# Kernel optimization log

Measured on AMD Instinct MI355X. Metric: run time of the kernel, lower is better.

## Reference

```python
import jax, jax.numpy as jnp
import numpy as np
from jax import lax

N_CLS = 3
ALPHA = 2
NMS = True


def _make_level(key, B, A, D, H, W, P, counts):
    k1, k2, k3, k4, k5 = jax.random.split(key, 5)
    C = N_CLS * A
    logit = jax.random.normal(k1, (B, C, D, H, W), dtype=jnp.float32)
    # valid positive coords use d,h,w >= 1 so padded writes to (0,0,0,0) never collide
    a = jax.random.randint(k2, (B, P), 0, A)
    d = jax.random.randint(k3, (B, P), 1, D)
    h = jax.random.randint(k4, (B, P), 1, H)
    w = jax.random.randint(k5, (B, P), 1, W)
    labels = jax.random.randint(jax.random.fold_in(key, 7), (B, P), 0, N_CLS)
    valid = jnp.arange(P)[None, :] < jnp.asarray(counts)[:, None]  # [B,P]
    coord = jnp.stack([a, d, h, w], axis=-1)
    coord = jnp.where(valid[..., None], coord, -1).astype(jnp.int32)
    # ground-truth prob map: -1 = negative, class id (float) at positive voxels
    prob_gt = -jnp.ones((B, A, D, H, W), dtype=jnp.float32)
    cs = jnp.where(valid[..., None], coord, 0)
    b_idx = jnp.arange(B)[:, None]
    vals = jnp.where(valid, labels.astype(jnp.float32), -1.0)
    prob_gt = prob_gt.at[b_idx, cs[..., 0], cs[..., 1], cs[..., 2], cs[..., 3]].set(vals)
    return logit, prob_gt, coord


def setup_inputs() -> dict:
    key = jax.random.key(0)
    kA, kB = jax.random.split(key)
    logit0, prob_gt0, coord0 = _make_level(kA, 4, 3, 64, 64, 64, 128, [128, 64, 32, 0])
    logit1, prob_gt1, coord1 = _make_level(kB, 4, 3, 32, 32, 32, 128, [64, 16, 8, 128])
    weight_cls = jnp.array([1.0, 1.5, 2.0], dtype=jnp.float32)
    return {
        "logit0": logit0, "logit1": logit1,
        "prob_gt0": prob_gt0, "prob_gt1": prob_gt1,
        "coord0": coord0, "coord1": coord1,
        "weight_cls": weight_cls,
    }


def _level_loss(logit, prob_gt, coord_gt, weight_cls):
    B, C, D, H, W = logit.shape
    A = C // N_CLS
    logit = logit.reshape(B, N_CLS, A, D, H, W)
    logp = jax.nn.log_softmax(logit, axis=1)
    nll = -logp                      # [B,N_cls,A,D,H,W]
    prob = jnp.exp(logp)
    nll_neg = nll[:, 0]              # [B,A,D,H,W]
    prob_neg = prob[:, 0]
    negmask = (prob_gt == -1).astype(logit.dtype)
    if NMS:
        mp = lax.reduce_window(nll_neg, -jnp.inf, lax.max,
                               (1, 1, 3, 3, 3), (1, 1, 1, 1, 1),
                               [(0, 0), (0, 0), (1, 1), (1, 1), (1, 1)])
        negmask = negmask * lax.stop_gradient((mp == nll_neg).astype(logit.dtype))
    w_neg = (1.0 - lax.stop_gradient(prob_neg)) ** ALPHA * negmask
    loss_neg = jnp.sum(nll_neg * w_neg)
    count_neg = jnp.sum(w_neg)
    # positives: ragged coord gather, masked instead of per-sample python loop
    valid = coord_gt[:, :, 0] > -1                       # [B,P]
    c = jnp.where(valid[..., None], coord_gt, 0)         # safe coords
    a, d, h, w = c[..., 0], c[..., 1], c[..., 2], c[..., 3]
    b_idx = jnp.arange(B)[:, None]
    cls = prob_gt[b_idx, a, d, h, w].astype(jnp.int32)   # class id at positives
    cls = jnp.where(valid, cls, 0)
    p_t = prob[b_idx, cls, a, d, h, w]
    nll_t = nll[b_idx, cls, a, d, h, w]
    w_pos = ((1.0 - lax.stop_gradient(p_t)) ** ALPHA
             * weight_cls[cls] * valid.astype(logit.dtype))
    loss_pos = jnp.sum(nll_t * w_pos)
    count_pos = jnp.sum(w_pos)
    return loss_pos, loss_neg, count_pos, count_neg


def reference(logit0, logit1, prob_gt0, prob_gt1, coord0, coord1, weight_cls):
    lp0, ln0, cp0, cn0 = _level_loss(logit0, prob_gt0, coord0, weight_cls)
    lp1, ln1, cp1, cn1 = _level_loss(logit1, prob_gt1, coord1, weight_cls)
    return jnp.stack([lp0 + lp1, ln0 + ln1, cp0 + cp1, cn0 + cn1])
```

## Files before the change

kernel.cpp:

```cpp
#include <hip/hip_runtime.h>
#include <math.h>

#define NEG_INF (-INFINITY)

__device__ __forceinline__ float nll3(float l0, float l1, float l2) {
    float m = fmaxf(l0, fmaxf(l1, l2));
    float e0 = __expf(l0 - m);
    float e1 = __expf(l1 - m);
    float e2 = __expf(l2 - m);
    return __logf(e0 + e1 + e2) - (l0 - m);
}

#define S0 262144
#define S1 32768
#define N0 (12 * S0)
#define N1 (12 * S1)
#define N0_4 (N0 / 4)
#define N1_4 (N1 / 4)
#define P1_BLOCKS ((N0_4 + N1_4) / 256)

__global__ __launch_bounds__(256)
void nll_pass(const float* __restrict__ logit0,
              const float* __restrict__ logit1,
              float* __restrict__ nllws) {
    const int idx = blockIdx.x * 256 + threadIdx.x;
    if (idx < N0_4) {
        const int per = S0 / 4;
        const int ba = idx / per, r4 = idx % per;
        const int a = ba % 3, b = ba / 3;
        const float* p = logit0 + ((long)b * 9 + a) * S0 + (long)r4 * 4;
        float4 l0 = *(const float4*)p;
        float4 l1 = *(const float4*)(p + (long)3 * S0);
        float4 l2 = *(const float4*)(p + (long)6 * S0);
        float4 o;
        o.x = nll3(l0.x, l1.x, l2.x);
        o.y = nll3(l0.y, l1.y, l2.y);
        o.z = nll3(l0.z, l1.z, l2.z);
        o.w = nll3(l0.w, l1.w, l2.w);
        *(float4*)(nllws + (long)ba * S0 + (long)r4 * 4) = o;
    } else {
        const int j = idx - N0_4;
        const int per = S1 / 4;
        const int ba = j / per, r4 = j % per;
        const int a = ba % 3, b = ba / 3;
        const float* p = logit1 + ((long)b * 9 + a) * S1 + (long)r4 * 4;
        float4 l0 = *(const float4*)p;
        float4 l1 = *(const float4*)(p + (long)3 * S1);
        float4 l2 = *(const float4*)(p + (long)6 * S1);
        float4 o;
        o.x = nll3(l0.x, l1.x, l2.x);
        o.y = nll3(l0.y, l1.y, l2.y);
        o.z = nll3(l0.z, l1.z, l2.z);
        o.w = nll3(l0.w, l1.w, l2.w);
        *(float4*)(nllws + N0 + (long)ba * S1 + (long)r4 * 4) = o;
    }
}

template<int W, int NR, int TD, int D, int H>
__device__ void nms_strip(int uid, int lane,
                          const float* __restrict__ nlvl,
                          const float* __restrict__ pg,
                          float2* __restrict__ slot) {
    constexpr int LR = W / 4;
    constexpr int NI = NR + 2;
    constexpr int HG = H / NR;
    constexpr int DT = D / TD;
    const int q = lane % LR;
    const int g = lane / LR;

    int t = uid;
    const int hg = t % HG; t /= HG;
    const int dt = t % DT; t /= DT;
    const int ba = t;
    const int h0 = hg * NR, d0 = dt * TD;
    const int HW = H * W;
    const long S = (long)D * HW;
    const float* nb  = nlvl + (long)ba * S;
    const float* pgb = pg + (long)ba * S;

    const int jrow = h0 - 1 + g;
    const bool hv = (jrow >= 0) && (jrow < H) && (g < NI);
    const int hcl = min(max(jrow, 0), H - 1);
    const int rowoff = hcl * W + 4 * q;
    const int prowoff = (h0 + min(g, NR - 1)) * W + 4 * q;

    float4 nl[3]; bool vd[3]; float4 pq[3];
    nl[0] = *(const float4*)(nb + (long)max(d0 - 1, 0) * HW + rowoff);
    vd[0] = (d0 - 1 >= 0);
    nl[1] = *(const float4*)(nb + (long)d0 * HW + rowoff);
    vd[1] = true;
    nl[2] = make_float4(0.f, 0.f, 0.f, 0.f); vd[2] = false;
    pq[0] = pq[1] = pq[2] = make_float4(0.f, 0.f, 0.f, 0.f);

    float vm0[4], vm1[4], cc1[4];
#pragma unroll
    for (int i = 0; i < 4; ++i) { vm0[i] = NEG_INF; vm1[i] = NEG_INF; cc1[i] = 0.f; }

    float loss = 0.f, cnt = 0.f;

#pragma unroll
    for (int s = 0; s <= TD + 1; ++s) {
        if (s <= TD - 1) {
            const int pd = d0 + 1 + s;
            nl[(s + 2) % 3] = *(const float4*)(nb + (long)min(pd, D - 1) * HW + rowoff);
            vd[(s + 2) % 3] = (pd < D);
            pq[s % 3] = *(const float4*)(pgb + (long)(d0 + s) * HW + prowoff);
        }

        const float4 cv = nl[s % 3];
        const bool vv = vd[s % 3] && hv;
        float nvv[4];
        nvv[0] = vv ? cv.x : NEG_INF;
        nvv[1] = vv ? cv.y : NEG_INF;
        nvv[2] = vv ? cv.z : NEG_INF;
        nvv[3] = vv ? cv.w : NEG_INF;

        float le = __shfl(nvv[3], lane - 1);
        float re = __shfl(nvv[0], lane + 1);
        le = (q == 0)      ? NEG_INF : le;
        re = (q == LR - 1) ? NEG_INF : re;
        float rm[4];
        rm[0] = fmaxf(le,     fmaxf(nvv[0], nvv[1]));
        rm[1] = fmaxf(nvv[0], fmaxf(nvv[1], nvv[2]));
        rm[2] = fmaxf(nvv[1], fmaxf(nvv[2], nvv[3]));
        rm[3] = fmaxf(nvv[2], fmaxf(nvv[3], re));

        float rmA[4], rmB[4], ctr[4];
#pragma unroll
        for (int i = 0; i < 4; ++i) {
            rmA[i] = __shfl(rm[i],  lane + LR);
            rmB[i] = __shfl(rm[i],  lane + 2 * LR);
            ctr[i] = __shfl(nvv[i], lane + LR);
        }

        const float4 gp = pq[(s + 1) % 3];
        const float pgv[4] = {gp.x, gp.y, gp.z, gp.w};
#pragma unroll
        for (int i = 0; i < 4; ++i) {
            float hw2 = fmaxf(rm[i], fmaxf(rmA[i], rmB[i]));
            if (s >= 2 && g < NR && pgv[i] == -1.0f) {
                float mp = fmaxf(vm0[i], fmaxf(vm1[i], hw2));
                if (mp == cc1[i]) {
                    float pn = __expf(-cc1[i]);
                    float wn = (1.f - pn) * (1.f - pn);
                    loss += cc1[i] * wn;
                    cnt  += wn;
                }
            }
            vm0[i] = vm1[i]; vm1[i] = hw2; cc1[i] = ctr[i];
        }
    }

#pragma unroll
    for (int off = 32; off > 0; off >>= 1) {
        loss += __shfl_down(loss, off);
        cnt  += __shfl_down(cnt, off);
    }
    if (lane == 0) slot[uid] = make_float2(loss, cnt);
}

__device__ void pos_wave8(int sub, int lane,
                          const float* __restrict__ logit,
                          const float* __restrict__ prob_gt,
                          const int* __restrict__ coord,
                          const float* __restrict__ wcls,
                          float2* __restrict__ slot,
                          int D, int H, int W) {
    const int A = 3, P = 128;
    const long S = (long)D * H * W;
    const int i = sub * 64 + lane;
    const int b = i / P;
    const int* c = coord + (long)i * 4;
    const int a = c[0];
    float loss = 0.f, cnt = 0.f;
    if (a > -1) {
        const int d = c[1], h = c[2], w = c[3];
        const long s = ((long)d * H + h) * W + w;
        const int cls = (int)prob_gt[((long)b * A + a) * S + s];
        const float* lp = logit + ((long)b * 3 * A + a) * S + s;
        float l0 = lp[0];
        float l1 = lp[(long)A * S];
        float l2 = lp[2L * A * S];
        float m = fmaxf(l0, fmaxf(l1, l2));
        float e0 = __expf(l0 - m);
        float e1 = __expf(l1 - m);
        float e2 = __expf(l2 - m);
        float lsum = __logf(e0 + e1 + e2);
        float lc = (cls == 0) ? l0 : ((cls == 1) ? l1 : l2);
        float lpc = (lc - m) - lsum;
        float pt = __expf(lpc);
        float wp = (1.f - pt) * (1.f - pt) * wcls[cls];
        loss = (-lpc) * wp;
        cnt = wp;
    }
#pragma unroll
    for (int off = 32; off > 0; off >>= 1) {
        loss += __shfl_down(loss, off);
        cnt  += __shfl_down(cnt, off);
    }
    if (lane == 0) *slot = make_float2(loss, cnt);
}

#define NW0 3072
#define NW1 384
#define NWP 16
#define NSLOT_NEG (NW0 + NW1)
#define TOTAL_WAVES (NW0 + NW1 + NWP)

__global__ __launch_bounds__(256)
void nms_pass(const float* __restrict__ nllws,
              const float* __restrict__ logit0,
              const float* __restrict__ logit1,
              const float* __restrict__ pg0,
              const float* __restrict__ pg1,
              const int* __restrict__ coord0,
              const int* __restrict__ coord1,
              const float* __restrict__ wcls,
              float2* __restrict__ slots) {
    const int gw = blockIdx.x * 4 + (threadIdx.x >> 6);
    const int lane = threadIdx.x & 63;
    if (gw < NW0) {
        nms_strip<64, 2, 8, 64, 64>(gw, lane, nllws, pg0, slots);
    } else if (gw < NW0 + NW1) {
        nms_strip<32, 4, 8, 32, 32>(gw - NW0, lane, nllws + N0, pg1, slots + NW0);
    } else if (gw < NW0 + NW1 + 8) {
        const int sub = gw - NW0 - NW1;
        pos_wave8(sub, lane, logit0, pg0, coord0, wcls,
                  slots + NSLOT_NEG + sub, 64, 64, 64);
    } else {
        const int sub = gw - NW0 - NW1 - 8;
        pos_wave8(sub, lane, logit1, pg1, coord1, wcls,
                  slots + NSLOT_NEG + 8 + sub, 32, 32, 32);
    }
}

__global__ __launch_bounds__(1024)
void final_reduce(const float2* __restrict__ slots, float* __restrict__ out) {
    float ln = 0.f, cn = 0.f, lp = 0.f, cp = 0.f;
    for (int i = threadIdx.x; i < NSLOT_NEG; i += 1024) {
        float2 v = slots[i]; ln += v.x; cn += v.y;
    }
    if (threadIdx.x < NWP) {
        float2 v = slots[NSLOT_NEG + threadIdx.x]; lp = v.x; cp = v.y;
    }
#pragma unroll
    for (int off = 32; off > 0; off >>= 1) {
        ln += __shfl_down(ln, off); cn += __shfl_down(cn, off);
        lp += __shfl_down(lp, off); cp += __shfl_down(cp, off);
    }
    __shared__ float s[16][4];
    const int wv = threadIdx.x >> 6;
    if ((threadIdx.x & 63) == 0) {
        s[wv][0] = ln; s[wv][1] = cn; s[wv][2] = lp; s[wv][3] = cp;
    }
    __syncthreads();
    if (threadIdx.x == 0) {
        float a = 0.f, b = 0.f, c = 0.f, d = 0.f;
#pragma unroll
        for (int i = 0; i < 16; ++i) {
            a += s[i][0]; b += s[i][1]; c += s[i][2]; d += s[i][3];
        }
        out[0] = c;
        out[1] = a;
        out[2] = d;
        out[3] = b;
    }
}

extern "C" void kernel_launch(void* const* d_in, const int* in_sizes, int n_in,
                              void* d_out, int out_size, void* d_ws, size_t ws_size,
                              hipStream_t stream) {
    const float* logit0   = (const float*)d_in[0];
    const float* logit1   = (const float*)d_in[1];
    const float* prob_gt0 = (const float*)d_in[2];
    const float* prob_gt1 = (const float*)d_in[3];
    const int*   coord0   = (const int*)d_in[4];
    const int*   coord1   = (const int*)d_in[5];
    const float* wcls     = (const float*)d_in[6];
    float* out = (float*)d_out;

    float*  nllws = (float*)d_ws;
    float2* slots = (float2*)(nllws + N0 + N1);

    nll_pass<<<P1_BLOCKS, 256, 0, stream>>>(logit0, logit1, nllws);
    nms_pass<<<TOTAL_WAVES / 4, 256, 0, stream>>>(
        nllws, logit0, logit1, prob_gt0, prob_gt1, coord0, coord1, wcls, slots);
    final_reduce<<<1, 1024, 0, stream>>>(slots, out);
}
```

Measured before the change: 108.8 us.

## Fuse final reduction into NMS pass via last-block atomic counter

After: 123.5 us. +13.5%, slower.

```diff
diff --git a/kernel.cpp b/kernel.cpp
--- a/kernel.cpp
+++ b/kernel.cpp
@@ -17,155 +17,22 @@
 #define N1 (12 * S1)
 #define N0_4 (N0 / 4)
 #define N1_4 (N1 / 4)
-#define P1_BLOCKS ((N0_4 + N1_4) / 256)
-
-__global__ __launch_bounds__(256)
-void nll_pass(const float* __restrict__ logit0,
-              const float* __restrict__ logit1,
-              float* __restrict__ nllws) {
-    const int idx = blockIdx.x * 256 + threadIdx.x;
-    if (idx < N0_4) {
-        const int per = S0 / 4;
-        const int ba = idx / per, r4 = idx % per;
-        const int a = ba % 3, b = ba / 3;
-        const float* p = logit0 + ((long)b * 9 + a) * S0 + (long)r4 * 4;
-        float4 l0 = *(const float4*)p;
-        float4 l1 = *(const float4*)(p + (long)3 * S0);
-        float4 l2 = *(const float4*)(p + (long)6 * S0);
-        float4 o;
-        o.x = nll3(l0.x, l1.x, l2.x);
-        o.y = nll3(l0.y, l1.y, l2.y);
-        o.z = nll3(l0.z, l1.z, l2.z);
-        o.w = nll3(l0.w, l1.w, l2.w);
-        *(float4*)(nllws + (long)ba * S0 + (long)r4 * 4) = o;
-    } else {
-        const int j = idx - N0_4;
-        const int per = S1 / 4;
-        const int ba = j / per, r4 = j % per;
-        const int a = ba % 3, b = ba / 3;
-        const float* p = logit1 + ((long)b * 9 + a) * S1 + (long)r4 * 4;
-        float4 l0 = *(const float4*)p;
-        float4 l1 = *(const float4*)(p + (long)3 * S1);
-        float4 l2 = *(const float4*)(p + (long)6 * S1);
-        float4 o;
-        o.x = nll3(l0.x, l1.x, l2.x);
-        o.y = nll3(l0.y, l1.y, l2.y);
-        o.z = nll3(l0.z, l1.z, l2.z);
-        o.w = nll3(l0.w, l1.w, l2.w);
-        *(float4*)(nllws + N0 + (long)ba * S1 + (long)r4 * 4) = o;
-    }
-}
-
-template<int W, int NR, int TD, int D, int H>
-__device__ void nms_strip(int uid, int lane,
-                          const float* __restrict__ nlvl,
-                          const float* __restrict__ pg,
-                          float2* __restrict__ slot) {
-    constexpr int LR = W / 4;
-    constexpr int NI = NR + 2;
-    constexpr int HG = H / NR;
-    constexpr int DT = D / TD;
-    const int q = lane % LR;
-    const int g = lane / LR;
-
-    int t = uid;
-    const int hg = t % HG; t /= HG;
-    const int dt = t % DT; t /= DT;
-    const int ba = t;
-    const int h0 = hg * NR, d0 = dt * TD;
-    const int HW = H * W;
-    const long S = (long)D * HW;
-    const float* nb  = nlvl + (long)ba * S;
-    const float* pgb = pg + (long)ba * S;
-
-    const int jrow = h0 - 1 + g;
-    const bool hv = (jrow >= 0) && (jrow < H) && (g < NI);
-    const int hcl = min(max(jrow, 0), H - 1);
-    const int rowoff = hcl * W + 4 * q;
-    const int prowoff = (h0 + min(g, NR - 1)) * W + 4 * q;
-
-    float4 nl[3]; bool vd[3]; float4 pq[3];
-    nl[0] = *(const float4*)(nb + (long)max(d0 - 1, 0) * HW + rowoff);
-    vd[0] = (d0 - 1 >= 0);
-    nl[1] = *(const float4*)(nb + (long)d0 * HW + rowoff);
-    vd[1] = true;
-    nl[2] = make_float4(0.f, 0.f, 0.f, 0.f); vd[2] = false;
-    pq[0] = pq[1] = pq[2] = make_float4(0.f, 0.f, 0.f, 0.f);
-
-    float vm0[4], vm1[4], cc1[4];
-#pragma unroll
-    for (int i = 0; i < 4; ++i) { vm0[i] = NEG_INF; vm1[i] = NEG_INF; cc1[i] = 0.f; }
-
-    float loss = 0.f, cnt = 0.f;
-
-#pragma unroll
-    for (int s = 0; s <= TD + 1; ++s) {
-        if (s <= TD - 1) {
-            const int pd = d0 + 1 + s;
-            nl[(s + 2) % 3] = *(const float4*)(nb + (long)min(pd, D - 1) * HW + rowoff);
-            vd[(s + 2) % 3] = (pd < D);
-            pq[s % 3] = *(const float4*)(pgb + (long)(d0 + s) * HW + prowoff);
-        }
-
-        const float4 cv = nl[s % 3];
-        const bool vv = vd[s % 3] && hv;
-        float nvv[4];
-        nvv[0] = vv ? cv.x : NEG_INF;
-        nvv[1] = vv ? cv.y : NEG_INF;
-        nvv[2] = vv ? cv.z : NEG_INF;
-        nvv[3] = vv ? cv.w : NEG_INF;
-
-        float le = __shfl(nvv[3], lane - 1);
-        float re = __shfl(nvv[0], lane + 1);
-        le = (q == 0)      ? NEG_INF : le;
-        re = (q == LR - 1) ? NEG_INF : re;
-        float rm[4];
-        rm[0] = fmaxf(le,     fmaxf(nvv[0], nvv[1]));
-        rm[1] = fmaxf(nvv[0], fmaxf(nvv[1], nvv[2]));
-        rm[2] = fmaxf(nvv[1], fmaxf(nvv[2], nvv[3]));
-        rm[3] = fmaxf(nvv[2], fmaxf(nvv[3], re));
-
-        float rmA[4], rmB[4], ctr[4];
-#pragma unroll
-        for (int i = 0; i < 4; ++i) {
-            rmA[i] = __shfl(rm[i],  lane + LR);
-            rmB[i] = __shfl(rm[i],  lane + 2 * LR);
-            ctr[i] = __shfl(nvv[i], lane + LR);
-        }
-
-        const float4 gp = pq[(s + 1) % 3];
-        const float pgv[4] = {gp.x, gp.y, gp.z, gp.w};
-#pragma unroll
-        for (int i = 0; i < 4; ++i) {
-            float hw2 = fmaxf(rm[i], fmaxf(rmA[i], rmB[i]));
-            if (s >= 2 && g < NR && pgv[i] == -1.0f) {
-                float mp = fmaxf(vm0[i], fmaxf(vm1[i], hw2));
-                if (mp == cc1[i]) {
-                    float pn = __expf(-cc1[i]);
-                    float wn = (1.f - pn) * (1.f - pn);
-                    loss += cc1[i] * wn;
-                    cnt  += wn;
-                }
-            }
-            vm0[i] = vm1[i]; vm1[i] = hw2; cc1[i] = ctr[i];
-        }
-    }
-
-#pragma unroll
-    for (int off = 32; off > 0; off >>= 1) {
-        loss += __shfl_down(loss, off);
-        cnt  += __shfl_down(cnt, off);
-    }
-    if (lane == 0) slot[uid] = make_float2(loss, cnt);
-}
-
-__device__ void pos_wave8(int sub, int lane,
-                          const float* __restrict__ logit,
-                          const float* __restrict__ prob_gt,
-                          const int* __restrict__ coord,
-                          const float* __restrict__ wcls,
-                          float2* __restrict__ slot,
-                          int D, int H, int W) {
+#define P1_NLL_BLOCKS ((N0_4 + N1_4) / 256)
+#define P1_BLOCKS (P1_NLL_BLOCKS + 4)
+
+#define NW0 3072
+#define NW1 384
+#define P2_BLOCKS ((NW0 + NW1) / 4)
+#define NSLOT_NEG P2_BLOCKS
+#define NSLOT (NSLOT_NEG + 16)
+
+__device__ void pos_wave(int level, int sub, int lane,
+                         const float* __restrict__ logit,
+                         const float* __restrict__ prob_gt,
+                         const int* __restrict__ coord,
+                         const float* __restrict__ wcls,
+                         float2* __restrict__ slot,
+                         int D, int H, int W) {
     const int A = 3, P = 128;
     const long S = (long)D * H * W;
     const int i = sub * 64 + lane;
@@ -201,69 +68,226 @@
     if (lane == 0) *slot = make_float2(loss, cnt);
 }
 
-#define NW0 3072
-#define NW1 384
-#define NWP 16
-#define NSLOT_NEG (NW0 + NW1)
-#define TOTAL_WAVES (NW0 + NW1 + NWP)
+__global__ __launch_bounds__(256)
+void nll_pos_pass(const float* __restrict__ logit0,
+                  const float* __restrict__ logit1,
+                  const float* __restrict__ pg0,
+                  const float* __restrict__ pg1,
+                  const int* __restrict__ coord0,
+                  const int* __restrict__ coord1,
+                  const float* __restrict__ wcls,
+                  float* __restrict__ nllws,
+                  float2* __restrict__ slots,
+                  unsigned int* __restrict__ counter) {
+    if (blockIdx.x == 0 && threadIdx.x == 0) *counter = 0u;
+    if (blockIdx.x < P1_NLL_BLOCKS) {
+        const int idx = blockIdx.x * 256 + threadIdx.x;
+        if (idx < N0_4) {
+            const int per = S0 / 4;
+            const int ba = idx / per, r4 = idx % per;
+            const int a = ba % 3, b = ba / 3;
+            const float* p = logit0 + ((long)b * 9 + a) * S0 + (long)r4 * 4;
+            float4 l0 = *(const float4*)p;
+            float4 l1 = *(const float4*)(p + (long)3 * S0);
+            float4 l2 = *(const float4*)(p + (long)6 * S0);
+            float4 o;
+            o.x = nll3(l0.x, l1.x, l2.x);
+            o.y = nll3(l0.y, l1.y, l2.y);
+            o.z = nll3(l0.z, l1.z, l2.z);
+            o.w = nll3(l0.w, l1.w, l2.w);
+            *(float4*)(nllws + (long)ba * S0 + (long)r4 * 4) = o;
+        } else {
+            const int j = idx - N0_4;
+            const int per = S1 / 4;
+            const int ba = j / per, r4 = j % per;
+            const int a = ba % 3, b = ba / 3;
+            const float* p = logit1 + ((long)b * 9 + a) * S1 + (long)r4 * 4;
+            float4 l0 = *(const float4*)p;
+            float4 l1 = *(const float4*)(p + (long)3 * S1);
+            float4 l2 = *(const float4*)(p + (long)6 * S1);
+            float4 o;
+            o.x = nll3(l0.x, l1.x, l2.x);
+            o.y = nll3(l0.y, l1.y, l2.y);
+            o.z = nll3(l0.z, l1.z, l2.z);
+            o.w = nll3(l0.w, l1.w, l2.w);
+            *(float4*)(nllws + N0 + (long)ba * S1 + (long)r4 * 4) = o;
+        }
+    } else {
+        const int gp = (blockIdx.x - P1_NLL_BLOCKS) * 4 + (threadIdx.x >> 6);
+        const int lane = threadIdx.x & 63;
+        if (gp < 8)
+            pos_wave(0, gp, lane, logit0, pg0, coord0, wcls,
+                     slots + NSLOT_NEG + gp, 64, 64, 64);
+        else
+            pos_wave(1, gp - 8, lane, logit1, pg1, coord1, wcls,
+                     slots + NSLOT_NEG + gp, 32, 32, 32);
+    }
+}
+
+template<int W, int NR, int TD, int D, int H>
+__device__ void nms_strip(int uid, int lane,
+                          const float* __restrict__ nlvl,
+                          const float* __restrict__ pg,
+                          float& loss_out, float& cnt_out) {
+    constexpr int LR = W / 4;
+    constexpr int NI = NR + 2;
+    constexpr int HG = H / NR;
+    constexpr int DT = D / TD;
+    const int q = lane % LR;
+    const int g = lane / LR;
+
+    int t = uid;
+    const int hg = t % HG; t /= HG;
+    const int dt = t % DT; t /= DT;
+    const int ba = t;
+    const int h0 = hg * NR, d0 = dt * TD;
+    const int HW = H * W;
+    const long S = (long)D * HW;
+    const float* nb  = nlvl + (long)ba * S;
+    const float* pgb = pg + (long)ba * S;
+
+    const int jrow = h0 - 1 + g;
+    const bool hv = (jrow >= 0) && (jrow < H) && (g < NI);
+    const int hcl = min(max(jrow, 0), H - 1);
+    const int rowoff = hcl * W + 4 * q;
+    const int prowoff = (h0 + min(g, NR - 1)) * W + 4 * q;
+
+    float4 nl[3]; bool vd[3]; float4 pq[3];
+    nl[0] = *(const float4*)(nb + (long)max(d0 - 1, 0) * HW + rowoff);
+    vd[0] = (d0 - 1 >= 0);
+    nl[1] = *(const float4*)(nb + (long)d0 * HW + rowoff);
+    vd[1] = true;
+    nl[2] = make_float4(0.f, 0.f, 0.f, 0.f); vd[2] = false;
+    pq[0] = pq[1] = pq[2] = make_float4(0.f, 0.f, 0.f, 0.f);
+
+    float vm0[4], vm1[4], cc1[4];
+#pragma unroll
+    for (int i = 0; i < 4; ++i) { vm0[i] = NEG_INF; vm1[i] = NEG_INF; cc1[i] = 0.f; }
+
+    float loss = 0.f, cnt = 0.f;
+
+#pragma unroll
+    for (int s = 0; s <= TD + 1; ++s) {
+        if (s <= TD - 1) {
+            const int pd = d0 + 1 + s;
+            nl[(s + 2) % 3] = *(const float4*)(nb + (long)min(pd, D - 1) * HW + rowoff);
+            vd[(s + 2) % 3] = (pd < D);
+            pq[s % 3] = *(const float4*)(pgb + (long)(d0 + s) * HW + prowoff);
+        }
+
+        const float4 cv = nl[s % 3];
+        const bool vv = vd[s % 3] && hv;
+        float nvv[4];
+        nvv[0] = vv ? cv.x : NEG_INF;
+        nvv[1] = vv ? cv.y : NEG_INF;
+        nvv[2] = vv ? cv.z : NEG_INF;
+        nvv[3] = vv ? cv.w : NEG_INF;
+
+        float le = __shfl(nvv[3], lane - 1);
+        float re = __shfl(nvv[0], lane + 1);
+        le = (q == 0)      ? NEG_INF : le;
+        re = (q == LR - 1) ? NEG_INF : re;
+        float rm[4];
+        rm[0] = fmaxf(le,     fmaxf(nvv[0], nvv[1]));
+        rm[1] = fmaxf(nvv[0], fmaxf(nvv[1], nvv[2]));
+        rm[2] = fmaxf(nvv[1], fmaxf(nvv[2], nvv[3]));
+        rm[3] = fmaxf(nvv[2], fmaxf(nvv[3], re));
+
+        float rmA[4], rmB[4], ctr[4];
+#pragma unroll
+        for (int i = 0; i < 4; ++i) {
+            rmA[i] = __shfl(rm[i],  lane + LR);
+            rmB[i] = __shfl(rm[i],  lane + 2 * LR);
+            ctr[i] = __shfl(nvv[i], lane + LR);
+        }
+
+        const float4 gpv = pq[(s + 1) % 3];
+        const float pgv[4] = {gpv.x, gpv.y, gpv.z, gpv.w};
+#pragma unroll
+        for (int i = 0; i < 4; ++i) {
+            float hw2 = fmaxf(rm[i], fmaxf(rmA[i], rmB[i]));
+            if (s >= 2 && g < NR && pgv[i] == -1.0f) {
+                float mp = fmaxf(vm0[i], fmaxf(vm1[i], hw2));
+                if (mp == cc1[i]) {
+                    float pn = __expf(-cc1[i]);
+                    float wn = (1.f - pn) * (1.f - pn);
+                    loss += cc1[i] * wn;
+                    cnt  += wn;
+                }
+            }
+            vm0[i] = vm1[i]; vm1[i] = hw2; cc1[i] = ctr[i];
+        }
+    }
+
+#pragma unroll
+    for (int off = 32; off > 0; off >>= 1) {
+        loss += __shfl_down(loss, off);
+        cnt  += __shfl_down(cnt, off);
+    }
+    loss_out = loss; cnt_out = cnt;
+}
 
 __global__ __launch_bounds__(256)
 void nms_pass(const float* __restrict__ nllws,
-              const float* __restrict__ logit0,
-              const float* __restrict__ logit1,
               const float* __restrict__ pg0,
               const float* __restrict__ pg1,
-              const int* __restrict__ coord0,
-              const int* __restrict__ coord1,
-              const float* __restrict__ wcls,
-              float2* __restrict__ slots) {
+              float2* __restrict__ slots,
+              unsigned int* __restrict__ counter,
+              float* __restrict__ out) {
     const int gw = blockIdx.x * 4 + (threadIdx.x >> 6);
     const int lane = threadIdx.x & 63;
+    float loss, cnt;
     if (gw < NW0) {
-        nms_strip<64, 2, 8, 64, 64>(gw, lane, nllws, pg0, slots);
-    } else if (gw < NW0 + NW1) {
-        nms_strip<32, 4, 8, 32, 32>(gw - NW0, lane, nllws + N0, pg1, slots + NW0);
-    } else if (gw < NW0 + NW1 + 8) {
-        const int sub = gw - NW0 - NW1;
-        pos_wave8(sub, lane, logit0, pg0, coord0, wcls,
-                  slots + NSLOT_NEG + sub, 64, 64, 64);
+        nms_strip<64, 2, 8, 64, 64>(gw, lane, nllws, pg0, loss, cnt);
     } else {
-        const int sub = gw - NW0 - NW1 - 8;
-        pos_wave8(sub, lane, logit1, pg1, coord1, wcls,
-                  slots + NSLOT_NEG + 8 + sub, 32, 32, 32);
-    }
-}
-
-__global__ __launch_bounds__(1024)
-void final_reduce(const float2* __restrict__ slots, float* __restrict__ out) {
-    float ln = 0.f, cn = 0.f, lp = 0.f, cp = 0.f;
-    for (int i = threadIdx.x; i < NSLOT_NEG; i += 1024) {
-        float2 v = slots[i]; ln += v.x; cn += v.y;
-    }
-    if (threadIdx.x < NWP) {
-        float2 v = slots[NSLOT_NEG + threadIdx.x]; lp = v.x; cp = v.y;
-    }
-#pragma unroll
-    for (int off = 32; off > 0; off >>= 1) {
-        ln += __shfl_down(ln, off); cn += __shfl_down(cn, off);
-        lp += __shfl_down(lp, off); cp += __shfl_down(cp, off);
-    }
-    __shared__ float s[16][4];
+        nms_strip<32, 4, 8, 32, 32>(gw - NW0, lane, nllws + N0, pg1, loss, cnt);
+    }
+
+    __shared__ float sl[4], sc[4];
+    __shared__ int amLast;
     const int wv = threadIdx.x >> 6;
-    if ((threadIdx.x & 63) == 0) {
-        s[wv][0] = ln; s[wv][1] = cn; s[wv][2] = lp; s[wv][3] = cp;
-    }
+    if (lane == 0) { sl[wv] = loss; sc[wv] = cnt; }
     __syncthreads();
     if (threadIdx.x == 0) {
-        float a = 0.f, b = 0.f, c = 0.f, d = 0.f;
-#pragma unroll
-        for (int i = 0; i < 16; ++i) {
-            a += s[i][0]; b += s[i][1]; c += s[i][2]; d += s[i][3];
-        }
-        out[0] = c;
-        out[1] = a;
-        out[2] = d;
-        out[3] = b;
+        float L = sl[0] + sl[1] + sl[2] + sl[3];
+        float C = sc[0] + sc[1] + sc[2] + sc[3];
+        slots[blockIdx.x] = make_float2(L, C);
+        __threadfence();
+        unsigned prev = atomicAdd(counter, 1u);
+        amLast = (prev == P2_BLOCKS - 1);
+    }
+    __syncthreads();
+
+    if (amLast) {
+        __threadfence();
+        float ln = 0.f, cn = 0.f, lp = 0.f, cp = 0.f;
+        for (int i = threadIdx.x; i < NSLOT_NEG; i += 256) {
+            float2 v = slots[i]; ln += v.x; cn += v.y;
+        }
+        if (threadIdx.x < 16) {
+            float2 v = slots[NSLOT_NEG + threadIdx.x]; lp = v.x; cp = v.y;
+        }
+#pragma unroll
+        for (int off = 32; off > 0; off >>= 1) {
+            ln += __shfl_down(ln, off); cn += __shfl_down(cn, off);
+            lp += __shfl_down(lp, off); cp += __shfl_down(cp, off);
+        }
+        __shared__ float fr[4][4];
+        if (lane == 0) {
+            fr[wv][0] = ln; fr[wv][1] = cn; fr[wv][2] = lp; fr[wv][3] = cp;
+        }
+        __syncthreads();
+        if (threadIdx.x == 0) {
+            float a = 0.f, b = 0.f, c = 0.f, d = 0.f;
+#pragma unroll
+            for (int i = 0; i < 4; ++i) {
+                a += fr[i][0]; b += fr[i][1]; c += fr[i][2]; d += fr[i][3];
+            }
+            out[0] = c;
+            out[1] = a;
+            out[2] = d;
+            out[3] = b;
+        }
     }
 }
 
@@ -279,11 +303,13 @@
     const float* wcls     = (const float*)d_in[6];
     float* out = (float*)d_out;
 
-    float*  nllws = (float*)d_ws;
-    float2* slots = (float2*)(nllws + N0 + N1);
-
-    nll_pass<<<P1_BLOCKS, 256, 0, stream>>>(logit0, logit1, nllws);
-    nms_pass<<<TOTAL_WAVES / 4, 256, 0, stream>>>(
-        nllws, logit0, logit1, prob_gt0, prob_gt1, coord0, coord1, wcls, slots);
-    final_reduce<<<1, 1024, 0, stream>>>(slots, out);
-}
+    float*        nllws   = (float*)d_ws;
+    float2*       slots   = (float2*)(nllws + N0 + N1);
+    unsigned int* counter = (unsigned int*)(slots + NSLOT);
+
+    nll_pos_pass<<<P1_BLOCKS, 256, 0, stream>>>(
+        logit0, logit1, prob_gt0, prob_gt1, coord0, coord1, wcls,
+        nllws, slots, counter);
+    nms_pass<<<P2_BLOCKS, 256, 0, stream>>>(
+        nllws, prob_gt0, prob_gt1, slots, counter, out);
+}
```
